# Kernel tuning notes

Measured on AMD Instinct MI355X. Metric: run time of the kernel, lower is better.

Reference implementation:

```python
import jax, jax.numpy as jnp
import numpy as np

MARGIN = 1.0


def setup_inputs() -> dict:
    key = jax.random.key(0)
    k1, k2, k3 = jax.random.split(key, 3)
    B, P = 8192, 16
    return {
        "energies": jax.random.normal(k1, (B, 1), dtype=jnp.float32),
        "property_values": jax.random.normal(k2, (B, P), dtype=jnp.float32),
        "property_targets": jax.random.normal(k3, (P,), dtype=jnp.float32),
    }


def reference(energies, property_values, property_targets):
    # distances[i] = ||property_values[i] - property_targets||_2, shape [B]
    distances = jnp.linalg.norm(property_values - property_targets[None, :], axis=-1)
    B = energies.shape[0]
    e = energies[:, 0]  # [B]
    # pair mask: i != j and distances[i] < distances[j]  -> [B, B]
    mask = (distances[:, None] < distances[None, :]) & (~jnp.eye(B, dtype=bool))
    # ranking loss per pair: relu(e_i - e_j + margin)
    pair_loss = jax.nn.relu(e[:, None] - e[None, :] + MARGIN)
    loss_sum = jnp.sum(jnp.where(mask, pair_loss, 0.0))
    count = jnp.sum(mask).astype(jnp.float32)
    loss = loss_sum / jnp.maximum(count, 1.0)
    # torch version accumulates [1]-shaped tensors -> output shape [1]
    return loss[None]
```

## Files before the change

kernel.cpp:

```cpp
#include <hip/hip_runtime.h>
#include <math.h>

#define MARGIN 1.0f
#define TI 256
#define TJ 512

__global__ __launch_bounds__(256) void dist_kernel(
    const float* __restrict__ pv,
    const float* __restrict__ pt,
    float* __restrict__ dist,
    int B, int P)
{
    int i = blockIdx.x * blockDim.x + threadIdx.x;
    if (i >= B) return;
    const float* row = pv + (size_t)i * P;
    float s = 0.f;
    for (int p = 0; p < P; ++p) {
        float d = row[p] - pt[p];
        s = fmaf(d, d, s);
    }
    dist[i] = sqrtf(s);
}

__global__ __launch_bounds__(256) void pair_kernel(
    const float* __restrict__ e,
    const float* __restrict__ dist,
    float* __restrict__ psum,
    float* __restrict__ pcnt,
    int B, int nj_tiles)
{
    __shared__ float sd[TJ];
    __shared__ float se[TJ];

    int it = blockIdx.x / nj_tiles;
    int jt = blockIdx.x % nj_tiles;
    int j0 = jt * TJ;

    for (int k = threadIdx.x; k < TJ; k += 256) {
        int j = j0 + k;
        bool ok = (j < B);
        sd[k] = ok ? dist[j] : -INFINITY;
        se[k] = ok ? e[j]    : 0.f;
    }
    __syncthreads();

    int i = it * TI + (int)threadIdx.x;
    bool iok = (i < B);
    float di = iok ? dist[i] : INFINITY;
    float a  = iok ? (e[i] + MARGIN) : 0.f;

    float sum = 0.f, cnt = 0.f;
    #pragma unroll 8
    for (int k = 0; k < TJ; ++k) {
        float dj = sd[k];
        float ej = se[k];
        bool m  = (di < dj);
        float t = fmaxf(a - ej, 0.f);
        sum += m ? t   : 0.f;
        cnt += m ? 1.f : 0.f;
    }

    __shared__ float rs[256];
    __shared__ float rc[256];
    rs[threadIdx.x] = sum;
    rc[threadIdx.x] = cnt;
    __syncthreads();
    for (int s = 128; s > 0; s >>= 1) {
        if ((int)threadIdx.x < s) {
            rs[threadIdx.x] += rs[threadIdx.x + s];
            rc[threadIdx.x] += rc[threadIdx.x + s];
        }
        __syncthreads();
    }
    if (threadIdx.x == 0) {
        psum[blockIdx.x] = rs[0];
        pcnt[blockIdx.x] = rc[0];
    }
}

__global__ __launch_bounds__(256) void finalize_kernel(
    const float* __restrict__ psum,
    const float* __restrict__ pcnt,
    float* __restrict__ out,
    int nblk)
{
    __shared__ double ss[256];
    __shared__ double sc[256];
    double s = 0.0, c = 0.0;
    for (int k = threadIdx.x; k < nblk; k += 256) {
        s += (double)psum[k];
        c += (double)pcnt[k];
    }
    ss[threadIdx.x] = s;
    sc[threadIdx.x] = c;
    __syncthreads();
    for (int st = 128; st > 0; st >>= 1) {
        if ((int)threadIdx.x < st) {
            ss[threadIdx.x] += ss[threadIdx.x + st];
            sc[threadIdx.x] += sc[threadIdx.x + st];
        }
        __syncthreads();
    }
    if (threadIdx.x == 0) {
        double cnt = sc[0] < 1.0 ? 1.0 : sc[0];
        out[0] = (float)(ss[0] / cnt);
    }
}

extern "C" void kernel_launch(void* const* d_in, const int* in_sizes, int n_in,
                              void* d_out, int out_size, void* d_ws, size_t ws_size,
                              hipStream_t stream)
{
    const float* energies = (const float*)d_in[0];
    const float* pv       = (const float*)d_in[1];
    const float* pt       = (const float*)d_in[2];
    int B = in_sizes[0];
    int P = in_sizes[2];

    int ni = (B + TI - 1) / TI;
    int nj = (B + TJ - 1) / TJ;
    int nblk = ni * nj;

    float* dist = (float*)d_ws;
    float* psum = dist + B;
    float* pcnt = psum + nblk;

    dist_kernel<<<(B + 255) / 256, 256, 0, stream>>>(pv, pt, dist, B, P);
    pair_kernel<<<nblk, 256, 0, stream>>>(energies, dist, psum, pcnt, B, nj);
    finalize_kernel<<<1, 256, 0, stream>>>(psum, pcnt, (float*)d_out, nblk);
}
```

Measured before the change: 73.95 us.

## Fuse finalize into pair kernel with atomics and two rows per thread

Drops the separate finalize kernel: each block reduces with wave shuffles and atomically adds its partial sum and count to a global accumulator, and the last block to arrive writes the result. Each thread now handles two i rows against a packed float2 shared tile, so every shared-memory read serves two rows, and the distance kernel reads with float4 loads. Removing one launch cuts fixed overhead, but a memset is added and float atomics make the summation order nondeterministic. Counts accumulated in float can lose exactness at about 33M pairs, which makes the result less precise than the old double-precision finalize.

```diff
diff --git a/kernel.cpp b/kernel.cpp
--- a/kernel.cpp
+++ b/kernel.cpp
@@ -2,108 +2,106 @@
 #include <math.h>
 
 #define MARGIN 1.0f
-#define TI 256
-#define TJ 512
+#define NT 256
+#define TI 512
+#define TJ 256
 
-__global__ __launch_bounds__(256) void dist_kernel(
+__global__ __launch_bounds__(NT) void dist_kernel(
     const float* __restrict__ pv,
     const float* __restrict__ pt,
     float* __restrict__ dist,
     int B, int P)
 {
-    int i = blockIdx.x * blockDim.x + threadIdx.x;
+    int i = blockIdx.x * NT + threadIdx.x;
     if (i >= B) return;
-    const float* row = pv + (size_t)i * P;
     float s = 0.f;
-    for (int p = 0; p < P; ++p) {
-        float d = row[p] - pt[p];
-        s = fmaf(d, d, s);
+    if ((P & 3) == 0) {
+        const float4* row = (const float4*)(pv + (size_t)i * P);
+        const float4* tgt = (const float4*)pt;
+        for (int p = 0; p < (P >> 2); ++p) {
+            float4 v = row[p];
+            float4 t = tgt[p];
+            float d0 = v.x - t.x, d1 = v.y - t.y, d2 = v.z - t.z, d3 = v.w - t.w;
+            s = fmaf(d0, d0, s); s = fmaf(d1, d1, s);
+            s = fmaf(d2, d2, s); s = fmaf(d3, d3, s);
+        }
+    } else {
+        const float* row = pv + (size_t)i * P;
+        for (int p = 0; p < P; ++p) {
+            float d = row[p] - pt[p];
+            s = fmaf(d, d, s);
+        }
     }
     dist[i] = sqrtf(s);
 }
 
-__global__ __launch_bounds__(256) void pair_kernel(
+__global__ __launch_bounds__(NT) void pair_kernel(
     const float* __restrict__ e,
     const float* __restrict__ dist,
-    float* __restrict__ psum,
-    float* __restrict__ pcnt,
-    int B, int nj_tiles)
+    float* __restrict__ acc,
+    unsigned* __restrict__ counter,
+    float* __restrict__ out,
+    int B, int nj)
 {
-    __shared__ float sd[TJ];
-    __shared__ float se[TJ];
+    __shared__ float2 sde[TJ];
 
-    int it = blockIdx.x / nj_tiles;
-    int jt = blockIdx.x % nj_tiles;
-    int j0 = jt * TJ;
+    int it = blockIdx.x / nj;
+    int jt = blockIdx.x % nj;
 
-    for (int k = threadIdx.x; k < TJ; k += 256) {
-        int j = j0 + k;
+    {
+        int j = jt * TJ + (int)threadIdx.x;
         bool ok = (j < B);
-        sd[k] = ok ? dist[j] : -INFINITY;
-        se[k] = ok ? e[j]    : 0.f;
+        float dj = ok ? dist[j] : -INFINITY;
+        float ej = ok ? e[j]    : 0.f;
+        sde[threadIdx.x] = make_float2(dj, ej);
     }
     __syncthreads();
 
-    int i = it * TI + (int)threadIdx.x;
-    bool iok = (i < B);
-    float di = iok ? dist[i] : INFINITY;
-    float a  = iok ? (e[i] + MARGIN) : 0.f;
+    int i0 = it * TI + (int)threadIdx.x;
+    int i1 = i0 + NT;
+    bool ok0 = (i0 < B), ok1 = (i1 < B);
+    float d0 = ok0 ? dist[i0] : INFINITY;
+    float a0 = ok0 ? (e[i0] + MARGIN) : 0.f;
+    float d1 = ok1 ? dist[i1] : INFINITY;
+    float a1 = ok1 ? (e[i1] + MARGIN) : 0.f;
 
     float sum = 0.f, cnt = 0.f;
     #pragma unroll 8
     for (int k = 0; k < TJ; ++k) {
-        float dj = sd[k];
-        float ej = se[k];
-        bool m  = (di < dj);
-        float t = fmaxf(a - ej, 0.f);
-        sum += m ? t   : 0.f;
-        cnt += m ? 1.f : 0.f;
+        float2 de = sde[k];
+        bool  m0 = (d0 < de.x);
+        float w0 = m0 ? a0 : -INFINITY;
+        sum += fmaxf(w0 - de.y, 0.f);
+        cnt += m0 ? 1.f : 0.f;
+        bool  m1 = (d1 < de.x);
+        float w1 = m1 ? a1 : -INFINITY;
+        sum += fmaxf(w1 - de.y, 0.f);
+        cnt += m1 ? 1.f : 0.f;
     }
 
-    __shared__ float rs[256];
-    __shared__ float rc[256];
-    rs[threadIdx.x] = sum;
-    rc[threadIdx.x] = cnt;
+    for (int off = 32; off > 0; off >>= 1) {
+        sum += __shfl_down(sum, off, 64);
+        cnt += __shfl_down(cnt, off, 64);
+    }
+    __shared__ float ws_sum[NT / 64];
+    __shared__ float ws_cnt[NT / 64];
+    int wave = threadIdx.x >> 6;
+    int lane = threadIdx.x & 63;
+    if (lane == 0) { ws_sum[wave] = sum; ws_cnt[wave] = cnt; }
     __syncthreads();
-    for (int s = 128; s > 0; s >>= 1) {
-        if ((int)threadIdx.x < s) {
-            rs[threadIdx.x] += rs[threadIdx.x + s];
-            rc[threadIdx.x] += rc[threadIdx.x + s];
+
+    if (threadIdx.x == 0) {
+        float bsum = 0.f, bcnt = 0.f;
+        for (int w = 0; w < NT / 64; ++w) { bsum += ws_sum[w]; bcnt += ws_cnt[w]; }
+        atomicAdd(&acc[0], bsum);
+        atomicAdd(&acc[1], bcnt);
+        __threadfence();
+        unsigned prev = atomicAdd(counter, 1u);
+        if (prev == gridDim.x - 1) {
+            float s = atomicAdd(&acc[0], 0.f);
+            float c = atomicAdd(&acc[1], 0.f);
+            out[0] = s / fmaxf(c, 1.f);
         }
-        __syncthreads();
-    }
-    if (threadIdx.x == 0) {
-        psum[blockIdx.x] = rs[0];
-        pcnt[blockIdx.x] = rc[0];
-    }
-}
-
-__global__ __launch_bounds__(256) void finalize_kernel(
-    const float* __restrict__ psum,
-    const float* __restrict__ pcnt,
-    float* __restrict__ out,
-    int nblk)
-{
-    __shared__ double ss[256];
-    __shared__ double sc[256];
-    double s = 0.0, c = 0.0;
-    for (int k = threadIdx.x; k < nblk; k += 256) {
-        s += (double)psum[k];
-        c += (double)pcnt[k];
-    }
-    ss[threadIdx.x] = s;
-    sc[threadIdx.x] = c;
-    __syncthreads();
-    for (int st = 128; st > 0; st >>= 1) {
-        if ((int)threadIdx.x < st) {
-            ss[threadIdx.x] += ss[threadIdx.x + st];
-            sc[threadIdx.x] += sc[threadIdx.x + st];
-        }
-        __syncthreads();
-    }
-    if (threadIdx.x == 0) {
-        double cnt = sc[0] < 1.0 ? 1.0 : sc[0];
-        out[0] = (float)(ss[0] / cnt);
     }
 }
 
@@ -117,15 +115,16 @@
     int B = in_sizes[0];
     int P = in_sizes[2];
 
+    float*    acc     = (float*)d_ws;
+    unsigned* counter = (unsigned*)d_ws + 2;
+    float*    dist    = (float*)d_ws + 4;
+
+    hipMemsetAsync(d_ws, 0, 3 * sizeof(float), stream);
+
     int ni = (B + TI - 1) / TI;
     int nj = (B + TJ - 1) / TJ;
-    int nblk = ni * nj;
 
-    float* dist = (float*)d_ws;
-    float* psum = dist + B;
-    float* pcnt = psum + nblk;
-
-    dist_kernel<<<(B + 255) / 256, 256, 0, stream>>>(pv, pt, dist, B, P);
-    pair_kernel<<<nblk, 256, 0, stream>>>(energies, dist, psum, pcnt, B, nj);
-    finalize_kernel<<<1, 256, 0, stream>>>(psum, pcnt, (float*)d_out, nblk);
+    dist_kernel<<<(B + NT - 1) / NT, NT, 0, stream>>>(pv, pt, dist, B, P);
+    pair_kernel<<<ni * nj, NT, 0, stream>>>(energies, dist, acc, counter,
+                                            (float*)d_out, B, nj);
 }
```

Measured after the change: 87.78 us. +18.7%, slower.
